# Kernel tuning notes

Hardware: AMD Instinct MI355X
Metric: run time of the kernel (lower is better)

The kernel has to match this reference:

```python
import jax, jax.numpy as jnp
import numpy as np

SR = 48000          # sample_rate
N = 480000          # num_samples
MAX_DELAYS = 50     # max_num_delays


def one_pole_lowpass(x, a):
    # y[n] = a*x[n] + (1-a)*y[n-1], zero initial state (causal one-pole IIR)
    def step(y, xn):
        y = a * xn + (1.0 - a) * y
        return y, y
    _, ys = jax.lax.scan(step, jnp.zeros((), x.dtype), x)
    return ys


def one_pole_bandpass(x, low, high):
    # bandpass as difference of two one-pole lowpasses (high cutoff minus low cutoff)
    return one_pole_lowpass(x, high) - one_pole_lowpass(x, low)


def setup_inputs() -> dict:
    key = jax.random.key(0)
    k1, k2, k3 = jax.random.split(key, 3)
    input_signal = jax.random.normal(k1, (N,), dtype=jnp.float32)
    parameters = jax.random.uniform(k2, (5,), dtype=jnp.float32)
    delay_buffer = jax.random.normal(k3, (N,), dtype=jnp.float32)
    return {"input_signal": input_signal, "parameters": parameters, "delay_buffer": delay_buffer}


def reference(input_signal, parameters, delay_buffer):
    frequency = jnp.clip(parameters[0], 20.0, SR / 2)
    feedback = jnp.clip(parameters[1], 0.0, 0.99)
    filter_low = jnp.clip(parameters[2], 1e-7, 0.99)
    filter_high = jnp.clip(parameters[3], 1e-7, 0.99)
    gain = jnp.maximum(parameters[4], 1e-7)

    delay_length = jnp.clip(jnp.floor(SR / frequency), 1, N // 2).astype(jnp.int32)
    num_delays = jnp.minimum(N // delay_length, MAX_DELAYS)

    taps = jnp.arange(1, MAX_DELAYS, dtype=jnp.int32)          # i = 1..49
    shifts = taps * delay_length                                # delay_start per tap
    powers = feedback ** taps.astype(jnp.float32)               # feedback^i
    active = (taps < num_delays) & (shifts < N)                 # loop bounds / break mask

    # The one-pole bandpass is linear and causal, so filtering the truncated,
    # scaled segment equals scaling + truncating the filtered full buffer.
    filtered = one_pole_bandpass(delay_buffer, filter_low, filter_high)  # [N]

    rolled = jax.vmap(lambda s: jnp.roll(filtered, s))(shifts)  # [49, N]
    pos = jnp.arange(N)
    valid = (pos[None, :] >= shifts[:, None]) & active[:, None]
    contrib = jnp.where(valid, rolled * powers[:, None], 0.0)   # [49, N]

    output_signal = input_signal + contrib.sum(axis=0)
    return jnp.tanh(output_signal * gain)
```

## Files before the change

kernel.cpp:

```cpp
#include <hip/hip_runtime.h>
#include <math.h>

#define SRATE 48000
#define NN    480000
#define MAXD  50
#define TPB   256
#define NV4   (NN / 4)
#define NBLKS ((NV4 + TPB - 1) / TPB)

__device__ __forceinline__ float clampf(float v, float lo, float hi) {
    return fminf(fmaxf(v, lo), hi);
}

struct Params { float al, bl, ah, bh, feedback, gain; int dl, nd; };

__device__ __forceinline__ Params load_params(const float* __restrict__ p) {
    Params q;
    float freq  = clampf(p[0], 20.0f, (float)(SRATE / 2));
    q.feedback  = clampf(p[1], 0.0f, 0.99f);
    float alow  = clampf(p[2], 1e-7f, 0.99f);
    float ahigh = clampf(p[3], 1e-7f, 0.99f);
    q.gain      = fmaxf(p[4], 1e-7f);
    float dlf   = clampf(floorf((float)SRATE / freq), 1.0f, (float)(NN / 2));
    q.dl = (int)dlf;
    q.nd = min(NN / q.dl, MAXD);
    q.al = alow;  q.bl = 1.0f - alow;
    q.ah = ahigh; q.bh = 1.0f - ahigh;
    return q;
}

__device__ __forceinline__ void seg_affine(const float4& v, float a, float b,
                                           float& Y, float& D) {
    float t = v.x;
    t = fmaf(t, b, v.y);
    t = fmaf(t, b, v.z);
    t = fmaf(t, b, v.w);
    Y = a * t;
    float b2 = b * b;
    D = b2 * b2;
}

__device__ __forceinline__ void wave_scan(int lane, float& Yl, float& Dl,
                                          float& Yh, float& Dh) {
    for (int off = 1; off < 64; off <<= 1) {
        float pYl = __shfl_up(Yl, off), pDl = __shfl_up(Dl, off);
        float pYh = __shfl_up(Yh, off), pDh = __shfl_up(Dh, off);
        if (lane >= off) {
            Yl = fmaf(Dl, pYl, Yl); Dl *= pDl;
            Yh = fmaf(Dh, pYh, Yh); Dh *= pDh;
        }
    }
}

__global__ __launch_bounds__(TPB) void scan_agg(
    const float* __restrict__ x, const float* __restrict__ p,
    float4* __restrict__ blkAgg)
{
    Params q = load_params(p);
    int tid = threadIdx.x;
    int t = blockIdx.x * TPB + tid;
    float Yl = 0.f, Dl = 1.f, Yh = 0.f, Dh = 1.f;
    if (t < NV4) {
        float4 v = ((const float4*)x)[t];
        seg_affine(v, q.al, q.bl, Yl, Dl);
        seg_affine(v, q.ah, q.bh, Yh, Dh);
    }
    int lane = tid & 63;
    wave_scan(lane, Yl, Dl, Yh, Dh);

    __shared__ float wYl[4], wDl[4], wYh[4], wDh[4];
    int w = tid >> 6;
    if (lane == 63) { wYl[w] = Yl; wDl[w] = Dl; wYh[w] = Yh; wDh[w] = Dh; }
    __syncthreads();
    if (tid == TPB - 1) {
        float cYl = 0.f, cDl = 1.f, cYh = 0.f, cDh = 1.f;
        for (int j = 0; j < 3; ++j) {
            cYl = fmaf(wDl[j], cYl, wYl[j]); cDl *= wDl[j];
            cYh = fmaf(wDh[j], cYh, wYh[j]); cDh *= wDh[j];
        }
        float AYl = fmaf(Dl, cYl, Yl), ADl = Dl * cDl;
        float AYh = fmaf(Dh, cYh, Yh), ADh = Dh * cDh;
        blkAgg[blockIdx.x] = make_float4(AYl, ADl, AYh, ADh);
    }
}

__global__ __launch_bounds__(TPB) void scan_apply(
    const float* __restrict__ x, const float* __restrict__ p,
    const float4* __restrict__ blkAgg,
    float* __restrict__ filtered)
{
    Params q = load_params(p);
    int tid = threadIdx.x;
    int lane = tid & 63;
    int w = tid >> 6;
    int t = blockIdx.x * TPB + tid;
    bool valid = (t < NV4);

    float4 v = make_float4(0.f, 0.f, 0.f, 0.f);
    float Yl = 0.f, Dl = 1.f, Yh = 0.f, Dh = 1.f;
    if (valid) {
        v = ((const float4*)x)[t];
        seg_affine(v, q.al, q.bl, Yl, Dl);
        seg_affine(v, q.ah, q.bh, Yh, Dh);
    }
    wave_scan(lane, Yl, Dl, Yh, Dh);

    __shared__ float wYl[4], wDl[4], wYh[4], wDh[4];
    if (lane == 63) { wYl[w] = Yl; wDl[w] = Dl; wYh[w] = Yh; wDh[w] = Dh; }

    __shared__ float sYl[TPB], sDl[TPB], sYh[TPB], sDh[TPB];
    {
        int i2 = 2 * tid;
        float4 a0 = (i2     < NBLKS) ? blkAgg[i2]     : make_float4(0.f, 1.f, 0.f, 1.f);
        float4 a1 = (i2 + 1 < NBLKS) ? blkAgg[i2 + 1] : make_float4(0.f, 1.f, 0.f, 1.f);
        sYl[tid] = fmaf(a1.y, a0.x, a1.x); sDl[tid] = a1.y * a0.y;
        sYh[tid] = fmaf(a1.w, a0.z, a1.z); sDh[tid] = a1.w * a0.w;
    }
    __syncthreads();
    for (int off = 1; off < TPB; off <<= 1) {
        float cyl = sYl[tid], cdl = sDl[tid], cyh = sYh[tid], cdh = sDh[tid];
        float pyl = 0.f, pdl = 1.f, pyh = 0.f, pdh = 1.f;
        bool has = (tid >= off);
        if (has) { pyl = sYl[tid-off]; pdl = sDl[tid-off];
                   pyh = sYh[tid-off]; pdh = sDh[tid-off]; }
        __syncthreads();
        if (has) {
            sYl[tid] = fmaf(cdl, pyl, cyl); sDl[tid] = cdl * pdl;
            sYh[tid] = fmaf(cdh, pyh, cyh); sDh[tid] = cdh * pdh;
        }
        __syncthreads();
    }
    __shared__ float GYl_s, GYh_s;
    if (tid == 0) {
        int b = blockIdx.x;
        int qq = b >> 1;
        float GYl = 0.f, GDl = 1.f, GYh = 0.f, GDh = 1.f;
        if (qq > 0) { GYl = sYl[qq-1]; GDl = sDl[qq-1];
                      GYh = sYh[qq-1]; GDh = sDh[qq-1]; }
        if (b & 1) {
            float4 am = blkAgg[2 * qq];
            GYl = fmaf(am.y, GYl, am.x); GDl = am.y * GDl;
            GYh = fmaf(am.w, GYh, am.z); GDh = am.w * GDh;
        }
        (void)GDl; (void)GDh;
        GYl_s = GYl; GYh_s = GYh;
    }
    __syncthreads();

    float eYl = __shfl_up(Yl, 1), eDl = __shfl_up(Dl, 1);
    float eYh = __shfl_up(Yh, 1), eDh = __shfl_up(Dh, 1);
    if (lane == 0) { eYl = 0.f; eDl = 1.f; eYh = 0.f; eDh = 1.f; }
    float cYl = 0.f, cDl = 1.f, cYh = 0.f, cDh = 1.f;
    for (int j = 0; j < 3; ++j) {
        if (j < w) {
            cYl = fmaf(wDl[j], cYl, wYl[j]); cDl *= wDl[j];
            cYh = fmaf(wDh[j], cYh, wYh[j]); cDh *= wDh[j];
        }
    }
    float BYl = fmaf(eDl, cYl, eYl), BDl = eDl * cDl;
    float BYh = fmaf(eDh, cYh, eYh), BDh = eDh * cDh;
    float yl = fmaf(BDl, GYl_s, BYl);
    float yh = fmaf(BDh, GYh_s, BYh);

    if (valid) {
        float4 o;
        yl = fmaf(q.bl, yl, q.al * v.x); yh = fmaf(q.bh, yh, q.ah * v.x); o.x = yh - yl;
        yl = fmaf(q.bl, yl, q.al * v.y); yh = fmaf(q.bh, yh, q.ah * v.y); o.y = yh - yl;
        yl = fmaf(q.bl, yl, q.al * v.z); yh = fmaf(q.bh, yh, q.ah * v.z); o.z = yh - yl;
        yl = fmaf(q.bl, yl, q.al * v.w); yh = fmaf(q.bh, yh, q.ah * v.w); o.w = yh - yl;
        ((float4*)filtered)[t] = o;
    }
}

__global__ __launch_bounds__(TPB) void taps_kernel(
    const float* __restrict__ input, const float* __restrict__ p,
    const float* __restrict__ filtered, float* __restrict__ out)
{
    int t = blockIdx.x * TPB + threadIdx.x;
    if (t >= NV4) return;
    Params q = load_params(p);
    int n0 = t * 4;
    float4 in4 = ((const float4*)input)[t];
    float a0 = in4.x, a1 = in4.y, a2 = in4.z, a3 = in4.w;

    if ((q.dl & 3) == 0) {
        int m = min(q.nd - 1, n0 / q.dl);
        int s = q.dl;
        float wgt = q.feedback;
        for (int i = 1; i <= m; ++i) {
            float4 f = *(const float4*)(filtered + (n0 - s));
            a0 = fmaf(wgt, f.x, a0);
            a1 = fmaf(wgt, f.y, a1);
            a2 = fmaf(wgt, f.z, a2);
            a3 = fmaf(wgt, f.w, a3);
            s += q.dl;
            wgt *= q.feedback;
        }
    } else {
        int s = q.dl;
        float wgt = q.feedback;
        for (int i = 1; i < q.nd; ++i) {
            if (s > n0 + 3) break;
            int b0 = n0 - s, b1 = b0 + 1, b2 = b0 + 2, b3 = b0 + 3;
            float f0 = (b0 >= 0) ? filtered[b0] : 0.f;
            float f1 = (b1 >= 0) ? filtered[b1] : 0.f;
            float f2 = (b2 >= 0) ? filtered[b2] : 0.f;
            float f3 = (b3 >= 0) ? filtered[b3] : 0.f;
            a0 = fmaf(wgt, f0, a0);
            a1 = fmaf(wgt, f1, a1);
            a2 = fmaf(wgt, f2, a2);
            a3 = fmaf(wgt, f3, a3);
            s += q.dl;
            wgt *= q.feedback;
        }
    }
    float4 o;
    o.x = tanhf(a0 * q.gain);
    o.y = tanhf(a1 * q.gain);
    o.z = tanhf(a2 * q.gain);
    o.w = tanhf(a3 * q.gain);
    ((float4*)out)[t] = o;
}

extern "C" void kernel_launch(void* const* d_in, const int* in_sizes, int n_in,
                              void* d_out, int out_size, void* d_ws, size_t ws_size,
                              hipStream_t stream)
{
    const float* input  = (const float*)d_in[0];
    const float* params = (const float*)d_in[1];
    const float* dbuf   = (const float*)d_in[2];
    float* out = (float*)d_out;

    float* ws       = (float*)d_ws;
    float* filtered = ws;
    float4* blkAgg  = (float4*)(ws + NN);

    scan_agg  <<<NBLKS, TPB, 0, stream>>>(dbuf, params, blkAgg);
    scan_apply<<<NBLKS, TPB, 0, stream>>>(dbuf, params, blkAgg, filtered);
    taps_kernel<<<NBLKS, TPB, 0, stream>>>(input, params, filtered, out);
}
```

Before: 74.54 us.

## Fuse scan and tap kernels into one cooperative kernel with grid syncs

Merges the three launches (block aggregate, scan apply, taps) into one cooperative kernel that uses grid.sync between phases. The input segment stays in registers, so the second pass does not reload it and two kernel launch gaps are removed. The cross-block aggregate scan also changes from a shared-memory Hillis-Steele loop with many __syncthreads to wave shuffles followed by a small per-wave combine. In exchange it needs all NBLKS (469) blocks co-resident, which depends on occupancy (launch bounds ask for 2 blocks per CU), and it pays the cost of grid-wide barriers.

```diff
diff --git a/kernel.cpp b/kernel.cpp
--- a/kernel.cpp
+++ b/kernel.cpp
@@ -1,5 +1,8 @@
 #include <hip/hip_runtime.h>
+#include <hip/hip_cooperative_groups.h>
 #include <math.h>
+
+namespace cg = cooperative_groups;
 
 #define SRATE 48000
 #define NN    480000
@@ -52,49 +55,21 @@
     }
 }
 
-__global__ __launch_bounds__(TPB) void scan_agg(
-    const float* __restrict__ x, const float* __restrict__ p,
-    float4* __restrict__ blkAgg)
+__global__ __launch_bounds__(TPB, 2) void fused(
+    const float* __restrict__ x,
+    const float* __restrict__ input,
+    const float* __restrict__ p,
+    float4* __restrict__ blkAgg,
+    float* __restrict__ filtered,
+    float* __restrict__ out)
 {
+    cg::grid_group grid = cg::this_grid();
     Params q = load_params(p);
-    int tid = threadIdx.x;
-    int t = blockIdx.x * TPB + tid;
-    float Yl = 0.f, Dl = 1.f, Yh = 0.f, Dh = 1.f;
-    if (t < NV4) {
-        float4 v = ((const float4*)x)[t];
-        seg_affine(v, q.al, q.bl, Yl, Dl);
-        seg_affine(v, q.ah, q.bh, Yh, Dh);
-    }
-    int lane = tid & 63;
-    wave_scan(lane, Yl, Dl, Yh, Dh);
-
-    __shared__ float wYl[4], wDl[4], wYh[4], wDh[4];
-    int w = tid >> 6;
-    if (lane == 63) { wYl[w] = Yl; wDl[w] = Dl; wYh[w] = Yh; wDh[w] = Dh; }
-    __syncthreads();
-    if (tid == TPB - 1) {
-        float cYl = 0.f, cDl = 1.f, cYh = 0.f, cDh = 1.f;
-        for (int j = 0; j < 3; ++j) {
-            cYl = fmaf(wDl[j], cYl, wYl[j]); cDl *= wDl[j];
-            cYh = fmaf(wDh[j], cYh, wYh[j]); cDh *= wDh[j];
-        }
-        float AYl = fmaf(Dl, cYl, Yl), ADl = Dl * cDl;
-        float AYh = fmaf(Dh, cYh, Yh), ADh = Dh * cDh;
-        blkAgg[blockIdx.x] = make_float4(AYl, ADl, AYh, ADh);
-    }
-}
-
-__global__ __launch_bounds__(TPB) void scan_apply(
-    const float* __restrict__ x, const float* __restrict__ p,
-    const float4* __restrict__ blkAgg,
-    float* __restrict__ filtered)
-{
-    Params q = load_params(p);
-    int tid = threadIdx.x;
-    int lane = tid & 63;
-    int w = tid >> 6;
-    int t = blockIdx.x * TPB + tid;
-    bool valid = (t < NV4);
+    const int tid  = threadIdx.x;
+    const int lane = tid & 63;
+    const int w    = tid >> 6;
+    const int t    = blockIdx.x * TPB + tid;
+    const bool valid = (t < NV4);
 
     float4 v = make_float4(0.f, 0.f, 0.f, 0.f);
     float Yl = 0.f, Dl = 1.f, Yh = 0.f, Dh = 1.f;
@@ -107,29 +82,42 @@
 
     __shared__ float wYl[4], wDl[4], wYh[4], wDh[4];
     if (lane == 63) { wYl[w] = Yl; wDl[w] = Dl; wYh[w] = Yh; wDh[w] = Dh; }
-
-    __shared__ float sYl[TPB], sDl[TPB], sYh[TPB], sDh[TPB];
+    __syncthreads();
+    if (tid == TPB - 1) {
+        float cYl = 0.f, cDl = 1.f, cYh = 0.f, cDh = 1.f;
+        for (int j = 0; j < 3; ++j) {
+            cYl = fmaf(wDl[j], cYl, wYl[j]); cDl *= wDl[j];
+            cYh = fmaf(wDh[j], cYh, wYh[j]); cDh *= wDh[j];
+        }
+        blkAgg[blockIdx.x] = make_float4(fmaf(Dl, cYl, Yl), Dl * cDl,
+                                         fmaf(Dh, cYh, Yh), Dh * cDh);
+    }
+    grid.sync();
+
+    float aYl = 0.f, aDl = 1.f, aYh = 0.f, aDh = 1.f;
     {
         int i2 = 2 * tid;
         float4 a0 = (i2     < NBLKS) ? blkAgg[i2]     : make_float4(0.f, 1.f, 0.f, 1.f);
         float4 a1 = (i2 + 1 < NBLKS) ? blkAgg[i2 + 1] : make_float4(0.f, 1.f, 0.f, 1.f);
-        sYl[tid] = fmaf(a1.y, a0.x, a1.x); sDl[tid] = a1.y * a0.y;
-        sYh[tid] = fmaf(a1.w, a0.z, a1.z); sDh[tid] = a1.w * a0.w;
-    }
-    __syncthreads();
-    for (int off = 1; off < TPB; off <<= 1) {
-        float cyl = sYl[tid], cdl = sDl[tid], cyh = sYh[tid], cdh = sDh[tid];
-        float pyl = 0.f, pdl = 1.f, pyh = 0.f, pdh = 1.f;
-        bool has = (tid >= off);
-        if (has) { pyl = sYl[tid-off]; pdl = sDl[tid-off];
-                   pyh = sYh[tid-off]; pdh = sDh[tid-off]; }
-        __syncthreads();
-        if (has) {
-            sYl[tid] = fmaf(cdl, pyl, cyl); sDl[tid] = cdl * pdl;
-            sYh[tid] = fmaf(cdh, pyh, cyh); sDh[tid] = cdh * pdh;
-        }
-        __syncthreads();
-    }
+        aYl = fmaf(a1.y, a0.x, a1.x); aDl = a1.y * a0.y;
+        aYh = fmaf(a1.w, a0.z, a1.z); aDh = a1.w * a0.w;
+    }
+    wave_scan(lane, aYl, aDl, aYh, aDh);
+    __shared__ float uYl[4], uDl[4], uYh[4], uDh[4];
+    if (lane == 63) { uYl[w] = aYl; uDl[w] = aDl; uYh[w] = aYh; uDh[w] = aDh; }
+    __syncthreads();
+    {
+        float pYl = 0.f, pDl = 1.f, pYh = 0.f, pDh = 1.f;
+        for (int j = 0; j < 3; ++j) if (j < w) {
+            pYl = fmaf(uDl[j], pYl, uYl[j]); pDl *= uDl[j];
+            pYh = fmaf(uDh[j], pYh, uYh[j]); pDh *= uDh[j];
+        }
+        aYl = fmaf(aDl, pYl, aYl); aDl *= pDl;
+        aYh = fmaf(aDh, pYh, aYh); aDh *= pDh;
+    }
+    __shared__ float sYl[TPB], sDl[TPB], sYh[TPB], sDh[TPB];
+    sYl[tid] = aYl; sDl[tid] = aDl; sYh[tid] = aYh; sDh[tid] = aDh;
+    __syncthreads();
     __shared__ float GYl_s, GYh_s;
     if (tid == 0) {
         int b = blockIdx.x;
@@ -170,56 +158,51 @@
         yl = fmaf(q.bl, yl, q.al * v.w); yh = fmaf(q.bh, yh, q.ah * v.w); o.w = yh - yl;
         ((float4*)filtered)[t] = o;
     }
-}
-
-__global__ __launch_bounds__(TPB) void taps_kernel(
-    const float* __restrict__ input, const float* __restrict__ p,
-    const float* __restrict__ filtered, float* __restrict__ out)
-{
-    int t = blockIdx.x * TPB + threadIdx.x;
-    if (t >= NV4) return;
-    Params q = load_params(p);
-    int n0 = t * 4;
-    float4 in4 = ((const float4*)input)[t];
-    float a0 = in4.x, a1 = in4.y, a2 = in4.z, a3 = in4.w;
-
-    if ((q.dl & 3) == 0) {
-        int m = min(q.nd - 1, n0 / q.dl);
-        int s = q.dl;
-        float wgt = q.feedback;
-        for (int i = 1; i <= m; ++i) {
-            float4 f = *(const float4*)(filtered + (n0 - s));
-            a0 = fmaf(wgt, f.x, a0);
-            a1 = fmaf(wgt, f.y, a1);
-            a2 = fmaf(wgt, f.z, a2);
-            a3 = fmaf(wgt, f.w, a3);
-            s += q.dl;
-            wgt *= q.feedback;
-        }
-    } else {
-        int s = q.dl;
-        float wgt = q.feedback;
-        for (int i = 1; i < q.nd; ++i) {
-            if (s > n0 + 3) break;
-            int b0 = n0 - s, b1 = b0 + 1, b2 = b0 + 2, b3 = b0 + 3;
-            float f0 = (b0 >= 0) ? filtered[b0] : 0.f;
-            float f1 = (b1 >= 0) ? filtered[b1] : 0.f;
-            float f2 = (b2 >= 0) ? filtered[b2] : 0.f;
-            float f3 = (b3 >= 0) ? filtered[b3] : 0.f;
-            a0 = fmaf(wgt, f0, a0);
-            a1 = fmaf(wgt, f1, a1);
-            a2 = fmaf(wgt, f2, a2);
-            a3 = fmaf(wgt, f3, a3);
-            s += q.dl;
-            wgt *= q.feedback;
-        }
-    }
-    float4 o;
-    o.x = tanhf(a0 * q.gain);
-    o.y = tanhf(a1 * q.gain);
-    o.z = tanhf(a2 * q.gain);
-    o.w = tanhf(a3 * q.gain);
-    ((float4*)out)[t] = o;
+    grid.sync();
+
+    if (valid) {
+        int n0 = t * 4;
+        float4 in4 = ((const float4*)input)[t];
+        float a0 = in4.x, a1 = in4.y, a2 = in4.z, a3 = in4.w;
+
+        if ((q.dl & 3) == 0) {
+            int m = min(q.nd - 1, n0 / q.dl);
+            int s = q.dl;
+            float wgt = q.feedback;
+            for (int i = 1; i <= m; ++i) {
+                float4 f = *(const float4*)(filtered + (n0 - s));
+                a0 = fmaf(wgt, f.x, a0);
+                a1 = fmaf(wgt, f.y, a1);
+                a2 = fmaf(wgt, f.z, a2);
+                a3 = fmaf(wgt, f.w, a3);
+                s += q.dl;
+                wgt *= q.feedback;
+            }
+        } else {
+            int s = q.dl;
+            float wgt = q.feedback;
+            for (int i = 1; i < q.nd; ++i) {
+                if (s > n0 + 3) break;
+                int b0 = n0 - s, b1 = b0 + 1, b2 = b0 + 2, b3 = b0 + 3;
+                float f0 = (b0 >= 0) ? filtered[b0] : 0.f;
+                float f1 = (b1 >= 0) ? filtered[b1] : 0.f;
+                float f2 = (b2 >= 0) ? filtered[b2] : 0.f;
+                float f3 = (b3 >= 0) ? filtered[b3] : 0.f;
+                a0 = fmaf(wgt, f0, a0);
+                a1 = fmaf(wgt, f1, a1);
+                a2 = fmaf(wgt, f2, a2);
+                a3 = fmaf(wgt, f3, a3);
+                s += q.dl;
+                wgt *= q.feedback;
+            }
+        }
+        float4 o;
+        o.x = tanhf(a0 * q.gain);
+        o.y = tanhf(a1 * q.gain);
+        o.z = tanhf(a2 * q.gain);
+        o.w = tanhf(a3 * q.gain);
+        ((float4*)out)[t] = o;
+    }
 }
 
 extern "C" void kernel_launch(void* const* d_in, const int* in_sizes, int n_in,
@@ -235,7 +218,8 @@
     float* filtered = ws;
     float4* blkAgg  = (float4*)(ws + NN);
 
-    scan_agg  <<<NBLKS, TPB, 0, stream>>>(dbuf, params, blkAgg);
-    scan_apply<<<NBLKS, TPB, 0, stream>>>(dbuf, params, blkAgg, filtered);
-    taps_kernel<<<NBLKS, TPB, 0, stream>>>(input, params, filtered, out);
-}
+    void* args[] = { (void*)&dbuf, (void*)&input, (void*)&params,
+                     (void*)&blkAgg, (void*)&filtered, (void*)&out };
+    hipLaunchCooperativeKernel((void*)fused, dim3(NBLKS), dim3(TPB),
+                               args, 0, stream);
+}
```

New measurement: 173.1 us. +132.2%, slower.

## Fuse two-pass block scan into single-pass decoupled look-back scan

Applied to the files above, without the earlier changes.

Replaces the aggregate-then-apply pair of scan kernels with one kernel that publishes per-block aggregates and inclusive prefixes through flags and resolves its exclusive prefix with a wave-wide decoupled look-back. The goal is to avoid reading the delay buffer twice and to drop one kernel launch plus the block-level shared-memory scan over all aggregates. It adds a memset for the flags, spin-waits that rely on blocks being scheduled in order, and atomic traffic on the workspace.

```diff
diff --git a/kernel.cpp b/kernel.cpp
--- a/kernel.cpp
+++ b/kernel.cpp
@@ -7,6 +7,11 @@
 #define TPB   256
 #define NV4   (NN / 4)
 #define NBLKS ((NV4 + TPB - 1) / TPB)
+
+typedef unsigned long long u64;
+typedef unsigned int u32;
+
+#define SCOPE_AGENT __HIP_MEMORY_SCOPE_AGENT
 
 __device__ __forceinline__ float clampf(float v, float lo, float hi) {
     return fminf(fmaxf(v, lo), hi);
@@ -52,49 +57,27 @@
     }
 }
 
-__global__ __launch_bounds__(TPB) void scan_agg(
+__device__ __forceinline__ u64 packf2(float a, float b) {
+    return ((u64)__float_as_uint(b) << 32) | (u64)__float_as_uint(a);
+}
+__device__ __forceinline__ void unpackf2(u64 u, float& a, float& b) {
+    a = __uint_as_float((u32)u);
+    b = __uint_as_float((u32)(u >> 32));
+}
+
+__global__ __launch_bounds__(TPB) void scan_lookback(
     const float* __restrict__ x, const float* __restrict__ p,
-    float4* __restrict__ blkAgg)
+    u64* __restrict__ aggA, u64* __restrict__ aggB,
+    u64* __restrict__ prefA, u64* __restrict__ prefB,
+    u32* __restrict__ flags, float* __restrict__ filtered)
 {
     Params q = load_params(p);
-    int tid = threadIdx.x;
-    int t = blockIdx.x * TPB + tid;
-    float Yl = 0.f, Dl = 1.f, Yh = 0.f, Dh = 1.f;
-    if (t < NV4) {
-        float4 v = ((const float4*)x)[t];
-        seg_affine(v, q.al, q.bl, Yl, Dl);
-        seg_affine(v, q.ah, q.bh, Yh, Dh);
-    }
-    int lane = tid & 63;
-    wave_scan(lane, Yl, Dl, Yh, Dh);
-
-    __shared__ float wYl[4], wDl[4], wYh[4], wDh[4];
-    int w = tid >> 6;
-    if (lane == 63) { wYl[w] = Yl; wDl[w] = Dl; wYh[w] = Yh; wDh[w] = Dh; }
-    __syncthreads();
-    if (tid == TPB - 1) {
-        float cYl = 0.f, cDl = 1.f, cYh = 0.f, cDh = 1.f;
-        for (int j = 0; j < 3; ++j) {
-            cYl = fmaf(wDl[j], cYl, wYl[j]); cDl *= wDl[j];
-            cYh = fmaf(wDh[j], cYh, wYh[j]); cDh *= wDh[j];
-        }
-        float AYl = fmaf(Dl, cYl, Yl), ADl = Dl * cDl;
-        float AYh = fmaf(Dh, cYh, Yh), ADh = Dh * cDh;
-        blkAgg[blockIdx.x] = make_float4(AYl, ADl, AYh, ADh);
-    }
-}
-
-__global__ __launch_bounds__(TPB) void scan_apply(
-    const float* __restrict__ x, const float* __restrict__ p,
-    const float4* __restrict__ blkAgg,
-    float* __restrict__ filtered)
-{
-    Params q = load_params(p);
-    int tid = threadIdx.x;
-    int lane = tid & 63;
-    int w = tid >> 6;
-    int t = blockIdx.x * TPB + tid;
-    bool valid = (t < NV4);
+    const int tid  = threadIdx.x;
+    const int lane = tid & 63;
+    const int w    = tid >> 6;
+    const int b    = blockIdx.x;
+    const int t    = b * TPB + tid;
+    const bool valid = (t < NV4);
 
     float4 v = make_float4(0.f, 0.f, 0.f, 0.f);
     float Yl = 0.f, Dl = 1.f, Yh = 0.f, Dh = 1.f;
@@ -106,46 +89,90 @@
     wave_scan(lane, Yl, Dl, Yh, Dh);
 
     __shared__ float wYl[4], wDl[4], wYh[4], wDh[4];
+    __shared__ float sAgg[4];
+    __shared__ float exc[4];
     if (lane == 63) { wYl[w] = Yl; wDl[w] = Dl; wYh[w] = Yh; wDh[w] = Dh; }
-
-    __shared__ float sYl[TPB], sDl[TPB], sYh[TPB], sDh[TPB];
-    {
-        int i2 = 2 * tid;
-        float4 a0 = (i2     < NBLKS) ? blkAgg[i2]     : make_float4(0.f, 1.f, 0.f, 1.f);
-        float4 a1 = (i2 + 1 < NBLKS) ? blkAgg[i2 + 1] : make_float4(0.f, 1.f, 0.f, 1.f);
-        sYl[tid] = fmaf(a1.y, a0.x, a1.x); sDl[tid] = a1.y * a0.y;
-        sYh[tid] = fmaf(a1.w, a0.z, a1.z); sDh[tid] = a1.w * a0.w;
-    }
     __syncthreads();
-    for (int off = 1; off < TPB; off <<= 1) {
-        float cyl = sYl[tid], cdl = sDl[tid], cyh = sYh[tid], cdh = sDh[tid];
-        float pyl = 0.f, pdl = 1.f, pyh = 0.f, pdh = 1.f;
-        bool has = (tid >= off);
-        if (has) { pyl = sYl[tid-off]; pdl = sDl[tid-off];
-                   pyh = sYh[tid-off]; pdh = sDh[tid-off]; }
-        __syncthreads();
-        if (has) {
-            sYl[tid] = fmaf(cdl, pyl, cyl); sDl[tid] = cdl * pdl;
-            sYh[tid] = fmaf(cdh, pyh, cyh); sDh[tid] = cdh * pdh;
-        }
-        __syncthreads();
-    }
-    __shared__ float GYl_s, GYh_s;
-    if (tid == 0) {
-        int b = blockIdx.x;
-        int qq = b >> 1;
-        float GYl = 0.f, GDl = 1.f, GYh = 0.f, GDh = 1.f;
-        if (qq > 0) { GYl = sYl[qq-1]; GDl = sDl[qq-1];
-                      GYh = sYh[qq-1]; GDh = sDh[qq-1]; }
-        if (b & 1) {
-            float4 am = blkAgg[2 * qq];
-            GYl = fmaf(am.y, GYl, am.x); GDl = am.y * GDl;
-            GYh = fmaf(am.w, GYh, am.z); GDh = am.w * GDh;
-        }
-        (void)GDl; (void)GDh;
-        GYl_s = GYl; GYh_s = GYh;
+
+    if (tid == TPB - 1) {
+        float cYl = 0.f, cDl = 1.f, cYh = 0.f, cDh = 1.f;
+        for (int j = 0; j < 3; ++j) {
+            cYl = fmaf(wDl[j], cYl, wYl[j]); cDl *= wDl[j];
+            cYh = fmaf(wDh[j], cYh, wYh[j]); cDh *= wDh[j];
+        }
+        float AYl = fmaf(Dl, cYl, Yl), ADl = Dl * cDl;
+        float AYh = fmaf(Dh, cYh, Yh), ADh = Dh * cDh;
+        sAgg[0] = AYl; sAgg[1] = ADl; sAgg[2] = AYh; sAgg[3] = ADh;
+        if (b == 0) {
+            __hip_atomic_store(&prefA[0], packf2(AYl, ADl), __ATOMIC_RELAXED, SCOPE_AGENT);
+            __hip_atomic_store(&prefB[0], packf2(AYh, ADh), __ATOMIC_RELAXED, SCOPE_AGENT);
+            __hip_atomic_store(&flags[0], 2u, __ATOMIC_RELEASE, SCOPE_AGENT);
+        } else {
+            __hip_atomic_store(&aggA[b], packf2(AYl, ADl), __ATOMIC_RELAXED, SCOPE_AGENT);
+            __hip_atomic_store(&aggB[b], packf2(AYh, ADh), __ATOMIC_RELAXED, SCOPE_AGENT);
+            __hip_atomic_store(&flags[b], 1u, __ATOMIC_RELEASE, SCOPE_AGENT);
+        }
+    }
+
+    if (b == 0) {
+        if (tid == 0) { exc[0] = 0.f; exc[1] = 1.f; exc[2] = 0.f; exc[3] = 1.f; }
+    } else if (w == 0) {
+        float EYl = 0.f, EDl = 1.f, EYh = 0.f, EDh = 1.f;
+        int base = b - 1;
+        for (;;) {
+            int idx = base - lane;
+            bool have = (idx >= 0);
+            u32 f = 0;
+            if (have) {
+                f = __hip_atomic_load(&flags[idx], __ATOMIC_RELAXED, SCOPE_AGENT);
+                while (f == 0u)
+                    f = __hip_atomic_load(&flags[idx], __ATOMIC_RELAXED, SCOPE_AGENT);
+            }
+            __builtin_amdgcn_fence(__ATOMIC_ACQUIRE, "agent");
+            u64 m2 = __ballot(have && (f == 2u));
+            int F = (m2 != 0ull) ? (int)__builtin_ctzll(m2) : 63;
+            float vYl = 0.f, vDl = 1.f, vYh = 0.f, vDh = 1.f;
+            if (have && lane <= F) {
+                u64 uA, uB;
+                if (lane == F && f == 2u) {
+                    uA = __hip_atomic_load(&prefA[idx], __ATOMIC_RELAXED, SCOPE_AGENT);
+                    uB = __hip_atomic_load(&prefB[idx], __ATOMIC_RELAXED, SCOPE_AGENT);
+                } else {
+                    uA = __hip_atomic_load(&aggA[idx], __ATOMIC_RELAXED, SCOPE_AGENT);
+                    uB = __hip_atomic_load(&aggB[idx], __ATOMIC_RELAXED, SCOPE_AGENT);
+                }
+                unpackf2(uA, vYl, vDl);
+                unpackf2(uB, vYh, vDh);
+            }
+            for (int off = 1; off < 64; off <<= 1) {
+                float oYl = __shfl_down(vYl, off), oDl = __shfl_down(vDl, off);
+                float oYh = __shfl_down(vYh, off), oDh = __shfl_down(vDh, off);
+                if (lane + off < 64) {
+                    vYl = fmaf(vDl, oYl, vYl); vDl *= oDl;
+                    vYh = fmaf(vDh, oYh, vYh); vDh *= oDh;
+                }
+            }
+            if (lane == 0) {
+                EYl = fmaf(EDl, vYl, EYl); EDl *= vDl;
+                EYh = fmaf(EDh, vYh, EYh); EDh *= vDh;
+            }
+            if (m2 != 0ull) break;
+            base -= 64;
+        }
+        if (lane == 0) { exc[0] = EYl; exc[1] = EDl; exc[2] = EYh; exc[3] = EDh; }
     }
     __syncthreads();
+
+    const float EYl = exc[0], EDl = exc[1], EYh = exc[2], EDh = exc[3];
+
+    if (b > 0 && tid == 0) {
+        float AYl = sAgg[0], ADl = sAgg[1], AYh = sAgg[2], ADh = sAgg[3];
+        float PYl = fmaf(ADl, EYl, AYl), PDl = ADl * EDl;
+        float PYh = fmaf(ADh, EYh, AYh), PDh = ADh * EDh;
+        __hip_atomic_store(&prefA[b], packf2(PYl, PDl), __ATOMIC_RELAXED, SCOPE_AGENT);
+        __hip_atomic_store(&prefB[b], packf2(PYh, PDh), __ATOMIC_RELAXED, SCOPE_AGENT);
+        __hip_atomic_store(&flags[b], 2u, __ATOMIC_RELEASE, SCOPE_AGENT);
+    }
 
     float eYl = __shfl_up(Yl, 1), eDl = __shfl_up(Dl, 1);
     float eYh = __shfl_up(Yh, 1), eDh = __shfl_up(Dh, 1);
@@ -159,8 +186,8 @@
     }
     float BYl = fmaf(eDl, cYl, eYl), BDl = eDl * cDl;
     float BYh = fmaf(eDh, cYh, eYh), BDh = eDh * cDh;
-    float yl = fmaf(BDl, GYl_s, BYl);
-    float yh = fmaf(BDh, GYh_s, BYh);
+    float yl = fmaf(BDl, EYl, BYl);
+    float yh = fmaf(BDh, EYh, BYh);
 
     if (valid) {
         float4 o;
@@ -233,9 +260,14 @@
 
     float* ws       = (float*)d_ws;
     float* filtered = ws;
-    float4* blkAgg  = (float4*)(ws + NN);
-
-    scan_agg  <<<NBLKS, TPB, 0, stream>>>(dbuf, params, blkAgg);
-    scan_apply<<<NBLKS, TPB, 0, stream>>>(dbuf, params, blkAgg, filtered);
+    u64*   aggA     = (u64*)(ws + NN);
+    u64*   aggB     = aggA  + NBLKS;
+    u64*   prefA    = aggB  + NBLKS;
+    u64*   prefB    = prefA + NBLKS;
+    u32*   flags    = (u32*)(prefB + NBLKS);
+
+    hipMemsetAsync(flags, 0, NBLKS * sizeof(u32), stream);
+    scan_lookback<<<NBLKS, TPB, 0, stream>>>(dbuf, params, aggA, aggB,
+                                             prefA, prefB, flags, filtered);
     taps_kernel<<<NBLKS, TPB, 0, stream>>>(input, params, filtered, out);
 }
```

Measured after the change: 102.1 us. +37.0%, slower.

## Add warm-up truncated IIR fast path that fuses the filter scan into one pass

Applied to the files above, without the earlier changes.

When both one-pole decay factors make state older than 3072 samples negligible (b^3072 <= e^-20), each block recomputes its 1024 filtered outputs by scanning from 3072 samples earlier with zero initial state. This skips the cross-block aggregate and apply passes. The taps stage then runs in the second kernel, and the third launch becomes an early-exit stub. The cost is about 4x redundant reads and scan work on the filter input, plus a tiny truncation error. When the parameters make the fast path unsafe, the original exact three-kernel scan still runs.

```diff
diff --git a/kernel.cpp b/kernel.cpp
--- a/kernel.cpp
+++ b/kernel.cpp
@@ -7,6 +7,7 @@
 #define TPB   256
 #define NV4   (NN / 4)
 #define NBLKS ((NV4 + TPB - 1) / TPB)
+#define WARM  3072
 
 __device__ __forceinline__ float clampf(float v, float lo, float hi) {
     return fminf(fmaxf(v, lo), hi);
@@ -29,6 +30,11 @@
     return q;
 }
 
+__device__ __forceinline__ bool fast_path(const Params& q) {
+    float bmax = fmaxf(q.bl, q.bh);
+    return (float)WARM * logf(bmax) <= -20.0f;
+}
+
 __device__ __forceinline__ void seg_affine(const float4& v, float a, float b,
                                            float& Y, float& D) {
     float t = v.x;
@@ -52,133 +58,10 @@
     }
 }
 
-__global__ __launch_bounds__(TPB) void scan_agg(
-    const float* __restrict__ x, const float* __restrict__ p,
-    float4* __restrict__ blkAgg)
-{
-    Params q = load_params(p);
-    int tid = threadIdx.x;
-    int t = blockIdx.x * TPB + tid;
-    float Yl = 0.f, Dl = 1.f, Yh = 0.f, Dh = 1.f;
-    if (t < NV4) {
-        float4 v = ((const float4*)x)[t];
-        seg_affine(v, q.al, q.bl, Yl, Dl);
-        seg_affine(v, q.ah, q.bh, Yh, Dh);
-    }
-    int lane = tid & 63;
-    wave_scan(lane, Yl, Dl, Yh, Dh);
-
-    __shared__ float wYl[4], wDl[4], wYh[4], wDh[4];
-    int w = tid >> 6;
-    if (lane == 63) { wYl[w] = Yl; wDl[w] = Dl; wYh[w] = Yh; wDh[w] = Dh; }
-    __syncthreads();
-    if (tid == TPB - 1) {
-        float cYl = 0.f, cDl = 1.f, cYh = 0.f, cDh = 1.f;
-        for (int j = 0; j < 3; ++j) {
-            cYl = fmaf(wDl[j], cYl, wYl[j]); cDl *= wDl[j];
-            cYh = fmaf(wDh[j], cYh, wYh[j]); cDh *= wDh[j];
-        }
-        float AYl = fmaf(Dl, cYl, Yl), ADl = Dl * cDl;
-        float AYh = fmaf(Dh, cYh, Yh), ADh = Dh * cDh;
-        blkAgg[blockIdx.x] = make_float4(AYl, ADl, AYh, ADh);
-    }
-}
-
-__global__ __launch_bounds__(TPB) void scan_apply(
-    const float* __restrict__ x, const float* __restrict__ p,
-    const float4* __restrict__ blkAgg,
-    float* __restrict__ filtered)
-{
-    Params q = load_params(p);
-    int tid = threadIdx.x;
-    int lane = tid & 63;
-    int w = tid >> 6;
-    int t = blockIdx.x * TPB + tid;
-    bool valid = (t < NV4);
-
-    float4 v = make_float4(0.f, 0.f, 0.f, 0.f);
-    float Yl = 0.f, Dl = 1.f, Yh = 0.f, Dh = 1.f;
-    if (valid) {
-        v = ((const float4*)x)[t];
-        seg_affine(v, q.al, q.bl, Yl, Dl);
-        seg_affine(v, q.ah, q.bh, Yh, Dh);
-    }
-    wave_scan(lane, Yl, Dl, Yh, Dh);
-
-    __shared__ float wYl[4], wDl[4], wYh[4], wDh[4];
-    if (lane == 63) { wYl[w] = Yl; wDl[w] = Dl; wYh[w] = Yh; wDh[w] = Dh; }
-
-    __shared__ float sYl[TPB], sDl[TPB], sYh[TPB], sDh[TPB];
-    {
-        int i2 = 2 * tid;
-        float4 a0 = (i2     < NBLKS) ? blkAgg[i2]     : make_float4(0.f, 1.f, 0.f, 1.f);
-        float4 a1 = (i2 + 1 < NBLKS) ? blkAgg[i2 + 1] : make_float4(0.f, 1.f, 0.f, 1.f);
-        sYl[tid] = fmaf(a1.y, a0.x, a1.x); sDl[tid] = a1.y * a0.y;
-        sYh[tid] = fmaf(a1.w, a0.z, a1.z); sDh[tid] = a1.w * a0.w;
-    }
-    __syncthreads();
-    for (int off = 1; off < TPB; off <<= 1) {
-        float cyl = sYl[tid], cdl = sDl[tid], cyh = sYh[tid], cdh = sDh[tid];
-        float pyl = 0.f, pdl = 1.f, pyh = 0.f, pdh = 1.f;
-        bool has = (tid >= off);
-        if (has) { pyl = sYl[tid-off]; pdl = sDl[tid-off];
-                   pyh = sYh[tid-off]; pdh = sDh[tid-off]; }
-        __syncthreads();
-        if (has) {
-            sYl[tid] = fmaf(cdl, pyl, cyl); sDl[tid] = cdl * pdl;
-            sYh[tid] = fmaf(cdh, pyh, cyh); sDh[tid] = cdh * pdh;
-        }
-        __syncthreads();
-    }
-    __shared__ float GYl_s, GYh_s;
-    if (tid == 0) {
-        int b = blockIdx.x;
-        int qq = b >> 1;
-        float GYl = 0.f, GDl = 1.f, GYh = 0.f, GDh = 1.f;
-        if (qq > 0) { GYl = sYl[qq-1]; GDl = sDl[qq-1];
-                      GYh = sYh[qq-1]; GDh = sDh[qq-1]; }
-        if (b & 1) {
-            float4 am = blkAgg[2 * qq];
-            GYl = fmaf(am.y, GYl, am.x); GDl = am.y * GDl;
-            GYh = fmaf(am.w, GYh, am.z); GDh = am.w * GDh;
-        }
-        (void)GDl; (void)GDh;
-        GYl_s = GYl; GYh_s = GYh;
-    }
-    __syncthreads();
-
-    float eYl = __shfl_up(Yl, 1), eDl = __shfl_up(Dl, 1);
-    float eYh = __shfl_up(Yh, 1), eDh = __shfl_up(Dh, 1);
-    if (lane == 0) { eYl = 0.f; eDl = 1.f; eYh = 0.f; eDh = 1.f; }
-    float cYl = 0.f, cDl = 1.f, cYh = 0.f, cDh = 1.f;
-    for (int j = 0; j < 3; ++j) {
-        if (j < w) {
-            cYl = fmaf(wDl[j], cYl, wYl[j]); cDl *= wDl[j];
-            cYh = fmaf(wDh[j], cYh, wYh[j]); cDh *= wDh[j];
-        }
-    }
-    float BYl = fmaf(eDl, cYl, eYl), BDl = eDl * cDl;
-    float BYh = fmaf(eDh, cYh, eYh), BDh = eDh * cDh;
-    float yl = fmaf(BDl, GYl_s, BYl);
-    float yh = fmaf(BDh, GYh_s, BYh);
-
-    if (valid) {
-        float4 o;
-        yl = fmaf(q.bl, yl, q.al * v.x); yh = fmaf(q.bh, yh, q.ah * v.x); o.x = yh - yl;
-        yl = fmaf(q.bl, yl, q.al * v.y); yh = fmaf(q.bh, yh, q.ah * v.y); o.y = yh - yl;
-        yl = fmaf(q.bl, yl, q.al * v.z); yh = fmaf(q.bh, yh, q.ah * v.z); o.z = yh - yl;
-        yl = fmaf(q.bl, yl, q.al * v.w); yh = fmaf(q.bh, yh, q.ah * v.w); o.w = yh - yl;
-        ((float4*)filtered)[t] = o;
-    }
-}
-
-__global__ __launch_bounds__(TPB) void taps_kernel(
-    const float* __restrict__ input, const float* __restrict__ p,
+__device__ __forceinline__ void taps_body(
+    int t, const float* __restrict__ input, const Params& q,
     const float* __restrict__ filtered, float* __restrict__ out)
 {
-    int t = blockIdx.x * TPB + threadIdx.x;
-    if (t >= NV4) return;
-    Params q = load_params(p);
     int n0 = t * 4;
     float4 in4 = ((const float4*)input)[t];
     float a0 = in4.x, a1 = in4.y, a2 = in4.z, a3 = in4.w;
@@ -222,6 +105,189 @@
     ((float4*)out)[t] = o;
 }
 
+__global__ __launch_bounds__(TPB) void k1_filter_or_agg(
+    const float* __restrict__ x, const float* __restrict__ p,
+    float4* __restrict__ blkAgg, float* __restrict__ filtered)
+{
+    Params q = load_params(p);
+    const int tid  = threadIdx.x;
+    const int lane = tid & 63;
+    const int w    = tid >> 6;
+    const int b    = blockIdx.x;
+    __shared__ float wYl[4], wDl[4], wYh[4], wDh[4];
+
+    if (fast_path(q)) {
+        const int segBase = ((b * 1024 - WARM) >> 2) + tid * 4;
+        float4 v[4];
+        #pragma unroll
+        for (int k = 0; k < 4; ++k) {
+            int s = segBase + k;
+            v[k] = (s >= 0 && s < NV4) ? ((const float4*)x)[s]
+                                       : make_float4(0.f, 0.f, 0.f, 0.f);
+        }
+        float Yl = 0.f, Dl = 1.f, Yh = 0.f, Dh = 1.f;
+        #pragma unroll
+        for (int k = 0; k < 4; ++k) {
+            float y, d;
+            seg_affine(v[k], q.al, q.bl, y, d);
+            Yl = fmaf(d, Yl, y); Dl *= d;
+            seg_affine(v[k], q.ah, q.bh, y, d);
+            Yh = fmaf(d, Yh, y); Dh *= d;
+        }
+        wave_scan(lane, Yl, Dl, Yh, Dh);
+        if (lane == 63) { wYl[w] = Yl; wDl[w] = Dl; wYh[w] = Yh; wDh[w] = Dh; }
+        __syncthreads();
+        if (w == 3) {
+            float eYl = __shfl_up(Yl, 1), eDl = __shfl_up(Dl, 1);
+            float eYh = __shfl_up(Yh, 1), eDh = __shfl_up(Dh, 1);
+            if (lane == 0) { eYl = 0.f; eDl = 1.f; eYh = 0.f; eDh = 1.f; }
+            float cYl = 0.f, cDl = 1.f, cYh = 0.f, cDh = 1.f;
+            #pragma unroll
+            for (int j = 0; j < 3; ++j) {
+                cYl = fmaf(wDl[j], cYl, wYl[j]); cDl *= wDl[j];
+                cYh = fmaf(wDh[j], cYh, wYh[j]); cDh *= wDh[j];
+            }
+            float yl = fmaf(eDl, cYl, eYl);
+            float yh = fmaf(eDh, cYh, eYh);
+            #pragma unroll
+            for (int k = 0; k < 4; ++k) {
+                int s = segBase + k;
+                float4 vv = v[k], o;
+                yl = fmaf(q.bl, yl, q.al * vv.x); yh = fmaf(q.bh, yh, q.ah * vv.x); o.x = yh - yl;
+                yl = fmaf(q.bl, yl, q.al * vv.y); yh = fmaf(q.bh, yh, q.ah * vv.y); o.y = yh - yl;
+                yl = fmaf(q.bl, yl, q.al * vv.z); yh = fmaf(q.bh, yh, q.ah * vv.z); o.z = yh - yl;
+                yl = fmaf(q.bl, yl, q.al * vv.w); yh = fmaf(q.bh, yh, q.ah * vv.w); o.w = yh - yl;
+                if (s < NV4) ((float4*)filtered)[s] = o;
+            }
+        }
+        return;
+    }
+
+    int t = b * TPB + tid;
+    float Yl = 0.f, Dl = 1.f, Yh = 0.f, Dh = 1.f;
+    if (t < NV4) {
+        float4 v = ((const float4*)x)[t];
+        seg_affine(v, q.al, q.bl, Yl, Dl);
+        seg_affine(v, q.ah, q.bh, Yh, Dh);
+    }
+    wave_scan(lane, Yl, Dl, Yh, Dh);
+    if (lane == 63) { wYl[w] = Yl; wDl[w] = Dl; wYh[w] = Yh; wDh[w] = Dh; }
+    __syncthreads();
+    if (tid == TPB - 1) {
+        float cYl = 0.f, cDl = 1.f, cYh = 0.f, cDh = 1.f;
+        for (int j = 0; j < 3; ++j) {
+            cYl = fmaf(wDl[j], cYl, wYl[j]); cDl *= wDl[j];
+            cYh = fmaf(wDh[j], cYh, wYh[j]); cDh *= wDh[j];
+        }
+        float AYl = fmaf(Dl, cYl, Yl), ADl = Dl * cDl;
+        float AYh = fmaf(Dh, cYh, Yh), ADh = Dh * cDh;
+        blkAgg[b] = make_float4(AYl, ADl, AYh, ADh);
+    }
+}
+
+__global__ __launch_bounds__(TPB) void k2_taps_or_apply(
+    const float* __restrict__ x, const float* __restrict__ input,
+    const float* __restrict__ p, const float4* __restrict__ blkAgg,
+    float* __restrict__ filtered, float* __restrict__ out)
+{
+    Params q = load_params(p);
+    const int tid  = threadIdx.x;
+    const int lane = tid & 63;
+    const int w    = tid >> 6;
+    const int t    = blockIdx.x * TPB + tid;
+
+    if (fast_path(q)) {
+        if (t < NV4) taps_body(t, input, q, filtered, out);
+        return;
+    }
+
+    bool valid = (t < NV4);
+    float4 v = make_float4(0.f, 0.f, 0.f, 0.f);
+    float Yl = 0.f, Dl = 1.f, Yh = 0.f, Dh = 1.f;
+    if (valid) {
+        v = ((const float4*)x)[t];
+        seg_affine(v, q.al, q.bl, Yl, Dl);
+        seg_affine(v, q.ah, q.bh, Yh, Dh);
+    }
+    wave_scan(lane, Yl, Dl, Yh, Dh);
+
+    __shared__ float wYl[4], wDl[4], wYh[4], wDh[4];
+    if (lane == 63) { wYl[w] = Yl; wDl[w] = Dl; wYh[w] = Yh; wDh[w] = Dh; }
+
+    __shared__ float sYl[TPB], sDl[TPB], sYh[TPB], sDh[TPB];
+    {
+        int i2 = 2 * tid;
+        float4 a0 = (i2     < NBLKS) ? blkAgg[i2]     : make_float4(0.f, 1.f, 0.f, 1.f);
+        float4 a1 = (i2 + 1 < NBLKS) ? blkAgg[i2 + 1] : make_float4(0.f, 1.f, 0.f, 1.f);
+        sYl[tid] = fmaf(a1.y, a0.x, a1.x); sDl[tid] = a1.y * a0.y;
+        sYh[tid] = fmaf(a1.w, a0.z, a1.z); sDh[tid] = a1.w * a0.w;
+    }
+    __syncthreads();
+    for (int off = 1; off < TPB; off <<= 1) {
+        float cyl = sYl[tid], cdl = sDl[tid], cyh = sYh[tid], cdh = sDh[tid];
+        float pyl = 0.f, pdl = 1.f, pyh = 0.f, pdh = 1.f;
+        bool has = (tid >= off);
+        if (has) { pyl = sYl[tid-off]; pdl = sDl[tid-off];
+                   pyh = sYh[tid-off]; pdh = sDh[tid-off]; }
+        __syncthreads();
+        if (has) {
+            sYl[tid] = fmaf(cdl, pyl, cyl); sDl[tid] = cdl * pdl;
+            sYh[tid] = fmaf(cdh, pyh, cyh); sDh[tid] = cdh * pdh;
+        }
+        __syncthreads();
+    }
+    __shared__ float GYl_s, GYh_s;
+    if (tid == 0) {
+        int b = blockIdx.x;
+        int qq = b >> 1;
+        float GYl = 0.f, GDl = 1.f, GYh = 0.f, GDh = 1.f;
+        if (qq > 0) { GYl = sYl[qq-1]; GDl = sDl[qq-1];
+                      GYh = sYh[qq-1]; GDh = sDh[qq-1]; }
+        if (b & 1) {
+            float4 am = blkAgg[2 * qq];
+            GYl = fmaf(am.y, GYl, am.x); GDl = am.y * GDl;
+            GYh = fmaf(am.w, GYh, am.z); GDh = am.w * GDh;
+        }
+        (void)GDl; (void)GDh;
+        GYl_s = GYl; GYh_s = GYh;
+    }
+    __syncthreads();
+
+    float eYl = __shfl_up(Yl, 1), eDl = __shfl_up(Dl, 1);
+    float eYh = __shfl_up(Yh, 1), eDh = __shfl_up(Dh, 1);
+    if (lane == 0) { eYl = 0.f; eDl = 1.f; eYh = 0.f; eDh = 1.f; }
+    float cYl = 0.f, cDl = 1.f, cYh = 0.f, cDh = 1.f;
+    for (int j = 0; j < 3; ++j) {
+        if (j < w) {
+            cYl = fmaf(wDl[j], cYl, wYl[j]); cDl *= wDl[j];
+            cYh = fmaf(wDh[j], cYh, wYh[j]); cDh *= wDh[j];
+        }
+    }
+    float BYl = fmaf(eDl, cYl, eYl), BDl = eDl * cDl;
+    float BYh = fmaf(eDh, cYh, eYh), BDh = eDh * cDh;
+    float yl = fmaf(BDl, GYl_s, BYl);
+    float yh = fmaf(BDh, GYh_s, BYh);
+
+    if (valid) {
+        float4 o;
+        yl = fmaf(q.bl, yl, q.al * v.x); yh = fmaf(q.bh, yh, q.ah * v.x); o.x = yh - yl;
+        yl = fmaf(q.bl, yl, q.al * v.y); yh = fmaf(q.bh, yh, q.ah * v.y); o.y = yh - yl;
+        yl = fmaf(q.bl, yl, q.al * v.z); yh = fmaf(q.bh, yh, q.ah * v.z); o.z = yh - yl;
+        yl = fmaf(q.bl, yl, q.al * v.w); yh = fmaf(q.bh, yh, q.ah * v.w); o.w = yh - yl;
+        ((float4*)filtered)[t] = o;
+    }
+}
+
+__global__ __launch_bounds__(TPB) void k3_taps_or_stub(
+    const float* __restrict__ input, const float* __restrict__ p,
+    const float* __restrict__ filtered, float* __restrict__ out)
+{
+    Params q = load_params(p);
+    if (fast_path(q)) return;
+    int t = blockIdx.x * TPB + threadIdx.x;
+    if (t < NV4) taps_body(t, input, q, filtered, out);
+}
+
 extern "C" void kernel_launch(void* const* d_in, const int* in_sizes, int n_in,
                               void* d_out, int out_size, void* d_ws, size_t ws_size,
                               hipStream_t stream)
@@ -235,7 +301,8 @@
     float* filtered = ws;
     float4* blkAgg  = (float4*)(ws + NN);
 
-    scan_agg  <<<NBLKS, TPB, 0, stream>>>(dbuf, params, blkAgg);
-    scan_apply<<<NBLKS, TPB, 0, stream>>>(dbuf, params, blkAgg, filtered);
-    taps_kernel<<<NBLKS, TPB, 0, stream>>>(input, params, filtered, out);
-}
+    k1_filter_or_agg<<<NBLKS, TPB, 0, stream>>>(dbuf, params, blkAgg, filtered);
+    k2_taps_or_apply<<<NBLKS, TPB, 0, stream>>>(dbuf, input, params, blkAgg,
+                                                filtered, out);
+    k3_taps_or_stub <<<NBLKS, TPB, 0, stream>>>(input, params, filtered, out);
+}
```

New measurement: 74.38 us. No clear change (-0.2%).
